# Kernel optimization log

Measured on AMD Instinct MI355X. Metric: run time of the kernel, lower is better.

The kernel has to match this reference:

```python
import jax, jax.numpy as jnp
import numpy as np

S, X, G = 2048, 2048, 2
INPUT_SIZE = (3, 32, 32)
F = int(np.prod(INPUT_SIZE))


def setup_inputs() -> dict:
    key = jax.random.key(0)
    k1, k2, k3 = jax.random.split(key, 3)
    samples = jax.random.normal(k1, (S,) + INPUT_SIZE, dtype=jnp.float32)
    x = jax.random.normal(k2, (X,) + INPUT_SIZE, dtype=jnp.float32)
    # per-feature std per gradation, kept in [0.1, 1.0) like ranges_std scaling
    std = jax.random.uniform(k3, (G, F), dtype=jnp.float32, minval=0.1, maxval=1.0)
    return {"samples": samples, "x": x, "std": std}


def reference(samples, x, std):
    # samples: [S, C, H, W], x: [X, C, H, W], std: [G, F]
    G_, F_ = std.shape
    s = samples.reshape(samples.shape[0], F_)  # [S, F]
    xf = x.reshape(x.shape[0], F_)             # [X, F]
    w = 1.0 / (std * std)                       # [G, F] precision
    # per-gradation normalizer: -0.5*F*log(2pi) - sum_f log(std)
    const = -0.5 * F_ * jnp.log(2.0 * jnp.pi) - jnp.sum(jnp.log(std), axis=1)  # [G]
    # sum_f -0.5*((s-x)/std)^2 expanded: -0.5*(s^2 w - 2 s w x + x^2 w)
    A = jnp.einsum('sf,gf->gs', s * s, w)        # [G, S]
    C = jnp.einsum('xf,gf->gx', xf * xf, w)      # [G, X]
    B = jnp.einsum('sf,gf,xf->gsx', s, w, xf)    # [G, S, X] cross term
    logits = -0.5 * (A[:, :, None] - 2.0 * B + C[:, None, :]) + const[:, None, None]
    lp = jax.nn.logsumexp(logits, axis=2)        # over x (mixture components)
    lp = jax.nn.logsumexp(lp, axis=0)            # over gradations
    return lp - jnp.log(jnp.float32(x.shape[0] * G_))
```

## Files before the change

### kernel.cpp

```cpp
#include <hip/hip_runtime.h>
#include <math.h>
#include <stdint.h>

#define S_N 2048
#define X_N 2048
#define G_N 2
#define F_N 3072

#define TM 256
#define TN 128
#define BK 64
#define ITERS (F_N / BK)
#define NBUF 3

typedef __bf16 bf16;
typedef __bf16 bf16x4 __attribute__((ext_vector_type(4)));
typedef __bf16 bf16x8 __attribute__((ext_vector_type(8)));
typedef float f32x4 __attribute__((ext_vector_type(4)));
typedef int i32x4 __attribute__((ext_vector_type(4)));

__device__ __forceinline__ void gload_lds16(const bf16* g, void* l) {
  __builtin_amdgcn_global_load_lds(
      (const __attribute__((address_space(1))) void*)g,
      (__attribute__((address_space(3))) void*)l, 16, 0, 0);
}

__global__ __launch_bounds__(512) void k_prep(
    const float* __restrict__ samples, const float* __restrict__ xin,
    const float* __restrict__ stdv,
    bf16* __restrict__ U, bf16* __restrict__ V,
    float* __restrict__ A, float* __restrict__ C) {
  __shared__ float rlds[6432];
  int t = threadIdx.x;
  int bid = blockIdx.x;
  int lane = t & 63, wv = t >> 6;

  for (int i = t; i < 2 * F_N; i += 512) rlds[i] = 1.0f / stdv[i];

  float sl0 = 0.f, sl1 = 0.f;
  for (int i = t; i < F_N; i += 512) {
    sl0 += logf(stdv[i]);
    sl1 += logf(stdv[F_N + i]);
  }
  for (int o = 32; o; o >>= 1) { sl0 += __shfl_xor(sl0, o); sl1 += __shfl_xor(sl1, o); }
  if (lane == 0) { rlds[6400 + wv] = sl0; rlds[6408 + wv] = sl1; }
  __syncthreads();
  float t0 = 0.f, t1 = 0.f;
#pragma unroll
  for (int w2 = 0; w2 < 8; ++w2) { t0 += rlds[6400 + w2]; t1 += rlds[6408 + w2]; }
  const float KLOG = -0.5f * (float)F_N * 1.8378770664093453f;
  float c0 = KLOG - t0, c1 = KLOG - t1;

  int l32 = t & 31;
  int rr = bid * 16 + (t >> 5);
  bool isS = rr < S_N;
  int rx = isS ? rr : rr - S_N;
  const float* src = isS ? samples + (size_t)rx * F_N : xin + (size_t)rx * F_N;
  bf16* d0 = isS ? U + (size_t)rx * F_N : V + (size_t)rx * F_N;
  bf16* d1 = isS ? U + ((size_t)S_N + rx) * F_N : V + ((size_t)X_N + rx) * F_N;
  float a0 = 0.f, a1 = 0.f;
#pragma unroll 4
  for (int k = 0; k < 24; ++k) {
    int c4 = l32 + k * 32;
    float4 sv = ((const float4*)src)[c4];
    float4 q0 = ((const float4*)rlds)[c4];
    float4 q1 = ((const float4*)rlds)[768 + c4];
    bf16x4 b0, b1;
    b0[0] = (bf16)(sv.x * q0.x); b0[1] = (bf16)(sv.y * q0.y);
    b0[2] = (bf16)(sv.z * q0.z); b0[3] = (bf16)(sv.w * q0.w);
    b1[0] = (bf16)(sv.x * q1.x); b1[1] = (bf16)(sv.y * q1.y);
    b1[2] = (bf16)(sv.z * q1.z); b1[3] = (bf16)(sv.w * q1.w);
    float f0 = (float)b0[0], f1 = (float)b0[1], f2 = (float)b0[2], f3 = (float)b0[3];
    a0 += f0 * f0 + f1 * f1 + f2 * f2 + f3 * f3;
    float h0 = (float)b1[0], h1 = (float)b1[1], h2 = (float)b1[2], h3 = (float)b1[3];
    a1 += h0 * h0 + h1 * h1 + h2 * h2 + h3 * h3;
    ((bf16x4*)d0)[c4] = b0;
    ((bf16x4*)d1)[c4] = b1;
  }
  for (int o = 16; o; o >>= 1) { a0 += __shfl_xor(a0, o); a1 += __shfl_xor(a1, o); }
  if (l32 == 0) {
    if (isS) { A[rx] = a0 - 2.f * c0; A[S_N + rx] = a1 - 2.f * c1; }
    else     { C[rx] = a0;            C[X_N + rx] = a1; }
  }
}

__global__ __launch_bounds__(512, 2) void k_gemm(const bf16* __restrict__ U, const bf16* __restrict__ V,
                                                 const float* __restrict__ A, const float* __restrict__ C,
                                                 float* __restrict__ logits) {
  __shared__ i32x4 lds[NBUF * 2048 + NBUF * 1024];
  i32x4* ldsA = lds;
  i32x4* ldsB = lds + NBUF * 2048;

  int t = threadIdx.x;
  int g = blockIdx.z;
  int bm = blockIdx.y * TM;
  int bn = blockIdx.x * TN;

  const bf16* Ub = U + ((size_t)g * S_N + bm) * F_N;
  const bf16* Vb = V + ((size_t)g * X_N + bn) * F_N;

  int wave = t >> 6, lane = t & 63;
  int pos = wave >> 1;
  int kh = wave & 1;
  int wm = pos >> 1;
  int wn = pos & 1;
  int r = lane & 15, q = lane >> 4;
  int fr = (r >> 1) & 7;
  int ck = (kh * 4 + q) ^ fr;
  int abase = (wm * 128 + r) * 8;
  int bbase = (wn * 64 + r) * 8;

  int row0 = t >> 3;
  int gcc = (t & 7) ^ ((t >> 4) & 7);
  const bf16* gA[4];
  const bf16* gB[2];
#pragma unroll
  for (int j = 0; j < 4; ++j) gA[j] = Ub + (size_t)(row0 + j * 64) * F_N + gcc * 8;
#pragma unroll
  for (int j = 0; j < 2; ++j) gB[j] = Vb + (size_t)(row0 + j * 64) * F_N + gcc * 8;

  f32x4 acc[8][4] = {};
  bf16x8 afc[4], afn[4], bE[4], bO[4];

#pragma unroll
  for (int j = 0; j < 4; ++j) gload_lds16(gA[j], &ldsA[0 * 2048 + t + j * 512]);
#pragma unroll
  for (int j = 0; j < 2; ++j) gload_lds16(gB[j], &ldsB[0 * 1024 + t + j * 512]);
#pragma unroll
  for (int j = 0; j < 4; ++j) gload_lds16(gA[j] + BK, &ldsA[1 * 2048 + t + j * 512]);
#pragma unroll
  for (int j = 0; j < 2; ++j) gload_lds16(gB[j] + BK, &ldsB[1 * 1024 + t + j * 512]);
  asm volatile("s_waitcnt vmcnt(6)" ::: "memory");
  __builtin_amdgcn_s_barrier();
#pragma unroll
  for (int mi = 0; mi < 4; ++mi)
    afc[mi] = __builtin_bit_cast(bf16x8, ldsA[abase + mi * 128 + ck]);
#pragma unroll
  for (int ni = 0; ni < 4; ++ni)
    bE[ni] = __builtin_bit_cast(bf16x8, ldsB[bbase + ni * 128 + ck]);

  int cur = 0;

#define KTILE(IT, B_CUR, B_NXT)                                                  \
  {                                                                              \
    int k2 = (IT) + 2;                                                           \
    int pk = (k2 < ITERS ? k2 : 0) * BK;     \
    int stg = (cur >= 1) ? cur - 1 : 2;                           \
    int nxt = (cur == 2) ? 0 : cur + 1;                                          \
    const i32x4* LA  = ldsA + cur * 2048;                                        \
    const i32x4* LAn = ldsA + nxt * 2048;                                        \
    const i32x4* LBn = ldsB + nxt * 1024;                                        \
         \
    gload_lds16(gA[0] + pk, &ldsA[stg * 2048 + t]);                              \
    gload_lds16(gA[1] + pk, &ldsA[stg * 2048 + t + 512]);                        \
    gload_lds16(gA[2] + pk, &ldsA[stg * 2048 + t + 1024]);                       \
    __builtin_amdgcn_s_barrier();                                                \
    _Pragma("unroll")                                                            \
    for (int mi = 0; mi < 4; ++mi)                                               \
      afn[mi] = __builtin_bit_cast(bf16x8, LA[abase + (4 + mi) * 128 + ck]);     \
    __builtin_amdgcn_s_setprio(1);                                               \
    _Pragma("unroll")                                                            \
    for (int mi = 0; mi < 4; ++mi)                                               \
      _Pragma("unroll")                                                          \
      for (int ni = 0; ni < 4; ++ni)                                             \
        acc[mi][ni] = __builtin_amdgcn_mfma_f32_16x16x32_bf16(afc[mi], B_CUR[ni], acc[mi][ni], 0, 0, 0); \
    __builtin_amdgcn_s_setprio(0);                                               \
    __builtin_amdgcn_s_barrier();                                                \
     \
    gload_lds16(gA[3] + pk, &ldsA[stg * 2048 + t + 1536]);                       \
    gload_lds16(gB[0] + pk, &ldsB[stg * 1024 + t]);                              \
    gload_lds16(gB[1] + pk, &ldsB[stg * 1024 + t + 512]);                        \
     \
    asm volatile("s_waitcnt vmcnt(6)" ::: "memory");                             \
    __builtin_amdgcn_s_barrier();  \
    _Pragma("unroll")                                                            \
    for (int mi = 0; mi < 4; ++mi)                                               \
      afc[mi] = __builtin_bit_cast(bf16x8, LAn[abase + mi * 128 + ck]);          \
    _Pragma("unroll")                                                            \
    for (int ni = 0; ni < 4; ++ni)                                               \
      B_NXT[ni] = __builtin_bit_cast(bf16x8, LBn[bbase + ni * 128 + ck]);        \
    __builtin_amdgcn_s_setprio(1);                                               \
    _Pragma("unroll")                                                            \
    for (int mi = 0; mi < 4; ++mi)                                               \
      _Pragma("unroll")                                                          \
      for (int ni = 0; ni < 4; ++ni)                                             \
        acc[4 + mi][ni] = __builtin_amdgcn_mfma_f32_16x16x32_bf16(afn[mi], B_CUR[ni], acc[4 + mi][ni], 0, 0, 0); \
    __builtin_amdgcn_s_setprio(0);                                               \
    __builtin_amdgcn_s_barrier();                                                \
    cur = nxt;                                                                   \
  }

  for (int it0 = 0; it0 < ITERS; it0 += 2) {
    KTILE(it0,     bE, bO)
    KTILE(it0 + 1, bO, bE)
  }
#undef KTILE

  asm volatile("s_waitcnt vmcnt(0) lgkmcnt(0)" ::: "memory");
  __builtin_amdgcn_s_barrier();

  f32x4* scr = (f32x4*)lds;
  {
    f32x4* mw = scr + wave * 1024;
    if (kh == 0) {
#pragma unroll
      for (int mi = 0; mi < 8; ++mi)
#pragma unroll
        for (int nl = 0; nl < 2; ++nl)
          mw[(mi * 2 + nl) * 64 + lane] = acc[mi][2 + nl];
    } else {
#pragma unroll
      for (int mi = 0; mi < 8; ++mi)
#pragma unroll
        for (int nl = 0; nl < 2; ++nl)
          mw[(mi * 2 + nl) * 64 + lane] = acc[mi][nl];
    }
  }
  __syncthreads();
  {
    const f32x4* pw = scr + (wave ^ 1) * 1024;
    if (kh == 0) {
#pragma unroll
      for (int mi = 0; mi < 8; ++mi)
#pragma unroll
        for (int nl = 0; nl < 2; ++nl)
          acc[mi][nl] += pw[(mi * 2 + nl) * 64 + lane];
    } else {
#pragma unroll
      for (int mi = 0; mi < 8; ++mi)
#pragma unroll
        for (int nl = 0; nl < 2; ++nl)
          acc[mi][2 + nl] += pw[(mi * 2 + nl) * 64 + lane];
    }
  }

  const float* Ap = A + (size_t)g * S_N + bm + wm * 128;
  const float* Cp = C + (size_t)g * X_N + bn + wn * 64 + kh * 32;
  float cv[2];
  cv[0] = Cp[r]; cv[1] = Cp[16 + r];
#pragma unroll
  for (int mi = 0; mi < 8; ++mi) {
#pragma unroll
    for (int i = 0; i < 4; ++i) {
      int rowl = mi * 16 + q * 4 + i;
      float av = Ap[rowl];
      float* orow = logits + ((size_t)g * S_N + bm + wm * 128 + rowl) * X_N + bn + wn * 64 + kh * 32;
      if (kh == 0) {
        orow[r]      = acc[mi][0][i] - 0.5f * (av + cv[0]);
        orow[16 + r] = acc[mi][1][i] - 0.5f * (av + cv[1]);
      } else {
        orow[r]      = acc[mi][2][i] - 0.5f * (av + cv[0]);
        orow[16 + r] = acc[mi][3][i] - 0.5f * (av + cv[1]);
      }
    }
  }
}

__global__ void k_lse(const float* __restrict__ logits, float* __restrict__ out) {
  int s = blockIdx.x, t = threadIdx.x;
  const float4* p0 = (const float4*)(logits + (size_t)s * X_N);
  const float4* p1 = (const float4*)(logits + ((size_t)S_N + s) * X_N);
  float4 v[4];
  v[0] = p0[t]; v[1] = p0[t + 256];
  v[2] = p1[t]; v[3] = p1[t + 256];

  float m = v[0].x;
#pragma unroll
  for (int j = 0; j < 4; ++j) {
    m = fmaxf(m, v[j].x); m = fmaxf(m, v[j].y);
    m = fmaxf(m, v[j].z); m = fmaxf(m, v[j].w);
  }
  for (int o = 32; o; o >>= 1) m = fmaxf(m, __shfl_xor(m, o));
  __shared__ float redm[4];
  __shared__ float reds[4];
  int w = t >> 6, l = t & 63;
  if (l == 0) redm[w] = m;
  __syncthreads();
  m = fmaxf(fmaxf(redm[0], redm[1]), fmaxf(redm[2], redm[3]));

  float sum = 0.f;
#pragma unroll
  for (int j = 0; j < 4; ++j) {
    sum += expf(v[j].x - m) + expf(v[j].y - m) + expf(v[j].z - m) + expf(v[j].w - m);
  }
  for (int o = 32; o; o >>= 1) sum += __shfl_xor(sum, o);
  if (l == 0) reds[w] = sum;
  __syncthreads();
  if (t == 0) {
    float tot = reds[0] + reds[1] + reds[2] + reds[3];
    out[s] = m + logf(tot) - 8.317766166719343f;
  }
}

extern "C" void kernel_launch(void* const* d_in, const int* in_sizes, int n_in,
                              void* d_out, int out_size, void* d_ws, size_t ws_size,
                              hipStream_t stream) {
  const float* samples = (const float*)d_in[0];
  const float* xin     = (const float*)d_in[1];
  const float* stdv    = (const float*)d_in[2];
  float* out = (float*)d_out;

  char* ws = (char*)d_ws;
  size_t off = 0;
  bf16* U = (bf16*)(ws + off);        off += (size_t)G_N * S_N * F_N * 2;
  bf16* V = (bf16*)(ws + off);        off += (size_t)G_N * X_N * F_N * 2;
  float* logits = (float*)(ws + off); off += (size_t)G_N * S_N * X_N * 4;
  float* A = (float*)(ws + off);      off += (size_t)G_N * S_N * 4;
  float* C = (float*)(ws + off);      off += (size_t)G_N * X_N * 4;

  k_prep<<<dim3(256), dim3(512), 0, stream>>>(samples, xin, stdv, U, V, A, C);
  k_gemm<<<dim3(X_N / TN, S_N / TM, G_N), dim3(512), 0, stream>>>(U, V, A, C, logits);
  k_lse<<<dim3(S_N), dim3(256), 0, stream>>>(logits, out);
}
```

Baseline: 158.6 us.

## Simplify GEMM main loop to single-phase load, MFMA, barrier, fragment read

Replaces the two-half ping-pong K-loop with a single-phase loop. Each iteration now issues all six global-to-LDS loads, runs all 32 MFMAs on fragments already in registers, then waits once, takes one barrier, and reads the next tile's A and B fragments behind a sched_barrier. This cuts the barriers per K-tile from four to one and reduces register fragment buffers. The cost is that LDS fragment reads are no longer overlapped with the second half of the MFMA work, so LDS latency may be exposed at every iteration.

After: 159.8 us. No clear change (+0.8%).

```diff
diff --git a/kernel.cpp b/kernel.cpp
--- a/kernel.cpp
+++ b/kernel.cpp
@@ -120,7 +120,7 @@
   for (int j = 0; j < 2; ++j) gB[j] = Vb + (size_t)(row0 + j * 64) * F_N + gcc * 8;
 
   f32x4 acc[8][4] = {};
-  bf16x8 afc[4], afn[4], bE[4], bO[4];
+  bf16x8 af[8], bfr[4];
 
 #pragma unroll
   for (int j = 0; j < 4; ++j) gload_lds16(gA[j], &ldsA[0 * 2048 + t + j * 512]);
@@ -132,69 +132,50 @@
   for (int j = 0; j < 2; ++j) gload_lds16(gB[j] + BK, &ldsB[1 * 1024 + t + j * 512]);
   asm volatile("s_waitcnt vmcnt(6)" ::: "memory");
   __builtin_amdgcn_s_barrier();
-#pragma unroll
-  for (int mi = 0; mi < 4; ++mi)
-    afc[mi] = __builtin_bit_cast(bf16x8, ldsA[abase + mi * 128 + ck]);
+  __builtin_amdgcn_sched_barrier(0);
+#pragma unroll
+  for (int mi = 0; mi < 8; ++mi)
+    af[mi] = __builtin_bit_cast(bf16x8, ldsA[abase + mi * 128 + ck]);
 #pragma unroll
   for (int ni = 0; ni < 4; ++ni)
-    bE[ni] = __builtin_bit_cast(bf16x8, ldsB[bbase + ni * 128 + ck]);
+    bfr[ni] = __builtin_bit_cast(bf16x8, ldsB[bbase + ni * 128 + ck]);
 
   int cur = 0;
-
-#define KTILE(IT, B_CUR, B_NXT)                                                  \
-  {                                                                              \
-    int k2 = (IT) + 2;                                                           \
-    int pk = (k2 < ITERS ? k2 : 0) * BK;     \
-    int stg = (cur >= 1) ? cur - 1 : 2;                           \
-    int nxt = (cur == 2) ? 0 : cur + 1;                                          \
-    const i32x4* LA  = ldsA + cur * 2048;                                        \
-    const i32x4* LAn = ldsA + nxt * 2048;                                        \
-    const i32x4* LBn = ldsB + nxt * 1024;                                        \
-         \
-    gload_lds16(gA[0] + pk, &ldsA[stg * 2048 + t]);                              \
-    gload_lds16(gA[1] + pk, &ldsA[stg * 2048 + t + 512]);                        \
-    gload_lds16(gA[2] + pk, &ldsA[stg * 2048 + t + 1024]);                       \
-    __builtin_amdgcn_s_barrier();                                                \
-    _Pragma("unroll")                                                            \
-    for (int mi = 0; mi < 4; ++mi)                                               \
-      afn[mi] = __builtin_bit_cast(bf16x8, LA[abase + (4 + mi) * 128 + ck]);     \
-    __builtin_amdgcn_s_setprio(1);                                               \
-    _Pragma("unroll")                                                            \
-    for (int mi = 0; mi < 4; ++mi)                                               \
-      _Pragma("unroll")                                                          \
-      for (int ni = 0; ni < 4; ++ni)                                             \
-        acc[mi][ni] = __builtin_amdgcn_mfma_f32_16x16x32_bf16(afc[mi], B_CUR[ni], acc[mi][ni], 0, 0, 0); \
-    __builtin_amdgcn_s_setprio(0);                                               \
-    __builtin_amdgcn_s_barrier();                                                \
-     \
-    gload_lds16(gA[3] + pk, &ldsA[stg * 2048 + t + 1536]);                       \
-    gload_lds16(gB[0] + pk, &ldsB[stg * 1024 + t]);                              \
-    gload_lds16(gB[1] + pk, &ldsB[stg * 1024 + t + 512]);                        \
-     \
-    asm volatile("s_waitcnt vmcnt(6)" ::: "memory");                             \
-    __builtin_amdgcn_s_barrier();  \
-    _Pragma("unroll")                                                            \
-    for (int mi = 0; mi < 4; ++mi)                                               \
-      afc[mi] = __builtin_bit_cast(bf16x8, LAn[abase + mi * 128 + ck]);          \
-    _Pragma("unroll")                                                            \
-    for (int ni = 0; ni < 4; ++ni)                                               \
-      B_NXT[ni] = __builtin_bit_cast(bf16x8, LBn[bbase + ni * 128 + ck]);        \
-    __builtin_amdgcn_s_setprio(1);                                               \
-    _Pragma("unroll")                                                            \
-    for (int mi = 0; mi < 4; ++mi)                                               \
-      _Pragma("unroll")                                                          \
-      for (int ni = 0; ni < 4; ++ni)                                             \
-        acc[4 + mi][ni] = __builtin_amdgcn_mfma_f32_16x16x32_bf16(afn[mi], B_CUR[ni], acc[4 + mi][ni], 0, 0, 0); \
-    __builtin_amdgcn_s_setprio(0);                                               \
-    __builtin_amdgcn_s_barrier();                                                \
-    cur = nxt;                                                                   \
-  }
-
-  for (int it0 = 0; it0 < ITERS; it0 += 2) {
-    KTILE(it0,     bE, bO)
-    KTILE(it0 + 1, bO, bE)
-  }
-#undef KTILE
+  for (int it = 0; it < ITERS; ++it) {
+    int k2 = it + 2;
+    int pk = (k2 < ITERS ? k2 : 0) * BK;
+    int stg = (cur >= 1) ? cur - 1 : 2;
+    int nxt = (cur == 2) ? 0 : cur + 1;
+    const i32x4* LAn = ldsA + nxt * 2048;
+    const i32x4* LBn = ldsB + nxt * 1024;
+
+    gload_lds16(gA[0] + pk, &ldsA[stg * 2048 + t]);
+    gload_lds16(gA[1] + pk, &ldsA[stg * 2048 + t + 512]);
+    gload_lds16(gA[2] + pk, &ldsA[stg * 2048 + t + 1024]);
+    gload_lds16(gA[3] + pk, &ldsA[stg * 2048 + t + 1536]);
+    gload_lds16(gB[0] + pk, &ldsB[stg * 1024 + t]);
+    gload_lds16(gB[1] + pk, &ldsB[stg * 1024 + t + 512]);
+
+    __builtin_amdgcn_s_setprio(1);
+#pragma unroll
+    for (int mi = 0; mi < 8; ++mi)
+#pragma unroll
+      for (int ni = 0; ni < 4; ++ni)
+        acc[mi][ni] = __builtin_amdgcn_mfma_f32_16x16x32_bf16(af[mi], bfr[ni], acc[mi][ni], 0, 0, 0);
+    __builtin_amdgcn_s_setprio(0);
+
+    asm volatile("s_waitcnt vmcnt(6)" ::: "memory");
+    __builtin_amdgcn_s_barrier();
+    __builtin_amdgcn_sched_barrier(0);
+#pragma unroll
+    for (int mi = 0; mi < 8; ++mi)
+      af[mi] = __builtin_bit_cast(bf16x8, LAn[abase + mi * 128 + ck]);
+#pragma unroll
+    for (int ni = 0; ni < 4; ++ni)
+      bfr[ni] = __builtin_bit_cast(bf16x8, LBn[bbase + ni * 128 + ck]);
+
+    cur = nxt;
+  }
 
   asm volatile("s_waitcnt vmcnt(0) lgkmcnt(0)" ::: "memory");
   __builtin_amdgcn_s_barrier();
```
